# Performance work log

Hardware: AMD Instinct MI355X
Metric: run time of the kernel (lower is better)

## Reference

```python
import jax, jax.numpy as jnp
import numpy as np

NUM_EXPERTS = 64
TOPK = 2
N_TOKENS = 16384
DIM = 4096


def setup_inputs() -> dict:
    key = jax.random.key(0)
    k1, k2 = jax.random.split(key)
    x = jax.random.normal(k1, (N_TOKENS, DIM), dtype=jnp.float32)
    # gate weight, torch nn.Linear layout: [num_experts, dim], trunc-normal-ish small init
    W = jax.random.normal(k2, (NUM_EXPERTS, DIM), dtype=jnp.float32) * 0.02
    return {"x": x, "W": W}


def reference(x, W):
    # gate: logits = x @ W^T  -> [N, E]
    router_logits = x @ W.T
    # softmax computed in fp32 (matches dtype=torch.float32 in source)
    routing_weights = jax.nn.softmax(router_logits.astype(jnp.float32), axis=-1)
    # top-k experts per token
    top_w, selected_experts = jax.lax.top_k(routing_weights, TOPK)  # [N, k]
    top_w = top_w.astype(x.dtype)
    sel_flat = selected_experts.reshape(-1)  # [N*k]
    # histogram over experts (torch.histc with bins=num_experts)
    num_tokens_per_expert = jnp.bincount(sel_flat, length=NUM_EXPERTS)
    # stable argsort -> gather (permutation) indices grouping tokens by expert
    gather_indices = jnp.argsort(sel_flat, stable=True)
    return top_w.reshape(-1), gather_indices, num_tokens_per_expert
```

## Files before the change

### kernel.cpp

```cpp
#include <hip/hip_runtime.h>
#include <hip/hip_bf16.h>
#include <math.h>
#include <stdint.h>

#define N_TOKENS 16384
#define DIM 4096
#define NEXP 64

typedef const __attribute__((address_space(1))) void gvoid_t;
typedef __attribute__((address_space(3))) void svoid_t;
typedef short bf16x8 __attribute__((ext_vector_type(8)));
typedef float f32x4 __attribute__((ext_vector_type(4)));

constexpr int TOK_BLK = 32;

__device__ __forceinline__ unsigned short bf16_rn(float f) {
  unsigned u = __float_as_uint(f);
  u += 0x7fffu + ((u >> 16) & 1u);
  return (unsigned short)(u >> 16);
}
__device__ __forceinline__ float bf16_tof(unsigned short h) {
  return __uint_as_float(((unsigned)h) << 16);
}

__global__ __launch_bounds__(256) void k0_wsplit(const float* __restrict__ W,
                                                 unsigned short* __restrict__ hi,
                                                 unsigned short* __restrict__ lo,
                                                 int* __restrict__ cnt) {
  const int i = (blockIdx.x * 256 + threadIdx.x) * 4;
  const float4 f = *(const float4*)(W + i);
  ushort4 h, l;
  h.x = bf16_rn(f.x); l.x = bf16_rn(f.x - bf16_tof(h.x));
  h.y = bf16_rn(f.y); l.y = bf16_rn(f.y - bf16_tof(h.y));
  h.z = bf16_rn(f.z); l.z = bf16_rn(f.z - bf16_tof(h.z));
  h.w = bf16_rn(f.w); l.w = bf16_rn(f.w - bf16_tof(h.w));
  *(ushort4*)(hi + i) = h;
  *(ushort4*)(lo + i) = l;
  if (blockIdx.x < 8) {
    int4* c4 = (int4*)cnt;
    c4[blockIdx.x * 256 + threadIdx.x] = make_int4(0, 0, 0, 0);
  }
}

__global__ __launch_bounds__(256, 2) void k1_fused(
    const float* __restrict__ x, const unsigned short* __restrict__ Whi,
    const unsigned short* __restrict__ Wlo, float* __restrict__ topw,
    int* __restrict__ sel, int* __restrict__ cnt) {
  __shared__ unsigned short wh[2][NEXP * 64];
  __shared__ unsigned short wl[2][NEXP * 64];
  __shared__ float lg[TOK_BLK * 68];
  __shared__ int hist[NEXP];

  const int tid = threadIdx.x;
  const int lane = tid & 63;
  const int wid = __builtin_amdgcn_readfirstlane(tid >> 6);
  const int th = wid >> 1;
  const int eh = wid & 1;
  const int r = lane & 15;
  const int g = lane >> 4;
  const int tok0 = blockIdx.x * TOK_BLK;

  f32x4 acc[2] = {};

  auto stage_w = [&](unsigned short* hd, unsigned short* ld, int kc) {
#pragma unroll
    for (int q = 0; q < 2; ++q) {
      const int r0 = wid * 16 + q * 8;
      const int row = r0 + (lane >> 3);
      const int s = (lane & 7) ^ (row & 7);
      __builtin_amdgcn_global_load_lds((gvoid_t*)(Whi + (size_t)row * DIM + kc + 8 * s),
                                       (svoid_t*)(hd + r0 * 64), 16, 0, 0);
      __builtin_amdgcn_global_load_lds((gvoid_t*)(Wlo + (size_t)row * DIM + kc + 8 * s),
                                       (svoid_t*)(ld + r0 * 64), 16, 0, 0);
    }
  };

  const float* xrow = x + (size_t)(tok0 + th * 16 + r) * DIM + g * 8;

  auto xload = [&](float4* xd, int t) {
    const float* p = xrow + t * 64;
    xd[0] = *(const float4*)(p);
    xd[1] = *(const float4*)(p + 4);
    xd[2] = *(const float4*)(p + 32);
    xd[3] = *(const float4*)(p + 36);
  };

  auto body = [&](int t, float4* xc, float4* xn, unsigned short* whc,
                  unsigned short* wlc, unsigned short* whn, unsigned short* wln) {
    if (t + 1 < 64) {
      xload(xn, t + 1);
      stage_w(whn, wln, (t + 1) * 64);
    }
#pragma unroll
    for (int h = 0; h < 2; ++h) {
      const float fv[8] = {xc[2 * h].x, xc[2 * h].y, xc[2 * h].z, xc[2 * h].w,
                           xc[2 * h + 1].x, xc[2 * h + 1].y, xc[2 * h + 1].z,
                           xc[2 * h + 1].w};
      bf16x8 Ahi, Alo;
#pragma unroll
      for (int j = 0; j < 8; ++j) {
        const unsigned short hb = bf16_rn(fv[j]);
        Ahi[j] = (short)hb;
        Alo[j] = (short)bf16_rn(fv[j] - bf16_tof(hb));
      }
      const int ws = h * 4 + g;
#pragma unroll
      for (int nt = 0; nt < 2; ++nt) {
        const int wrow = eh * 32 + nt * 16 + r;
        const int wadr = wrow * 64 + 8 * (ws ^ (wrow & 7));
        const bf16x8 Bhi = *(const bf16x8*)(whc + wadr);
        const bf16x8 Blo = *(const bf16x8*)(wlc + wadr);
        acc[nt] = __builtin_amdgcn_mfma_f32_16x16x32_bf16(Ahi, Bhi, acc[nt], 0, 0, 0);
        acc[nt] = __builtin_amdgcn_mfma_f32_16x16x32_bf16(Alo, Bhi, acc[nt], 0, 0, 0);
        acc[nt] = __builtin_amdgcn_mfma_f32_16x16x32_bf16(Ahi, Blo, acc[nt], 0, 0, 0);
      }
    }
    __syncthreads();
  };

  float4 xA[4], xB[4];
  xload(xA, 0);
  stage_w(wh[0], wl[0], 0);
  __syncthreads();

  for (int tt = 0; tt < 64; tt += 2) {
    body(tt, xA, xB, wh[0], wl[0], wh[1], wl[1]);
    body(tt + 1, xB, xA, wh[1], wl[1], wh[0], wl[0]);
  }

  if (tid < NEXP) hist[tid] = 0;
#pragma unroll
  for (int nt = 0; nt < 2; ++nt)
#pragma unroll
    for (int rg = 0; rg < 4; ++rg)
      lg[(th * 16 + g * 4 + rg) * 68 + eh * 32 + nt * 16 + r] = acc[nt][rg];
  __syncthreads();

  if (tid < TOK_BLK) {
    const float* rowp = lg + tid * 68;
    float4 v[16];
#pragma unroll
    for (int c = 0; c < 16; ++c) v[c] = *(const float4*)(rowp + c * 4);

    float v0 = -INFINITY, v1 = -INFINITY;
    int i0 = 0, i1 = 0;
#define TOP2_STEP(val, idx)                                  \
  {                                                          \
    const float vv = (val);                                  \
    const int ee = (idx);                                    \
    if (vv > v0) { v1 = v0; i1 = i0; v0 = vv; i0 = ee; }     \
    else if (vv > v1) { v1 = vv; i1 = ee; }                  \
  }
#pragma unroll
    for (int c = 0; c < 16; ++c) {
      TOP2_STEP(v[c].x, c * 4 + 0);
      TOP2_STEP(v[c].y, c * 4 + 1);
      TOP2_STEP(v[c].z, c * 4 + 2);
      TOP2_STEP(v[c].w, c * 4 + 3);
    }
#undef TOP2_STEP

    float denom = 0.f;
#pragma unroll
    for (int c = 0; c < 16; ++c) {
      denom += expf(v[c].x - v0);
      denom += expf(v[c].y - v0);
      denom += expf(v[c].z - v0);
      denom += expf(v[c].w - v0);
    }
    const float w0 = 1.0f / denom;
    const float w1 = expf(v1 - v0) / denom;

    const int tk = tok0 + tid;
    topw[2 * tk + 0] = w0;
    topw[2 * tk + 1] = w1;
    sel[2 * tk + 0] = i0;
    sel[2 * tk + 1] = i1;
    atomicAdd(&hist[i0], 1);
    atomicAdd(&hist[i1], 1);
  }
  __syncthreads();
  if (tid < NEXP) {
    const int h = hist[tid];
    if (h) atomicAdd(&cnt[tid * 128 + (blockIdx.x >> 2)], h);
  }
}

__global__ void k3_scan(const int* __restrict__ cnt, int* __restrict__ cb,
                        float* __restrict__ counts_out) {
  __shared__ int tot[NEXP];
  const int e = threadIdx.x;
  const int4* row4 = (const int4*)(cnt + e * 128);
  int run = 0;
#pragma unroll
  for (int q = 0; q < 32; ++q) {
    const int4 v = row4[q];
    run += v.x + v.y + v.z + v.w;
  }
  tot[e] = run;
  counts_out[e] = (float)run;
  __syncthreads();
  int g = 0;
  for (int q = 0; q < e; ++q) g += tot[q];
  int r = g;
  for (int p = 0; p < 128; ++p) {
    cb[p * NEXP + e] = r;
    r += cnt[e * 128 + p];
  }
}

__global__ __launch_bounds__(256) void k4_scatter(const int* __restrict__ sel,
                                                  const int* __restrict__ cb,
                                                  float* __restrict__ gout) {
  __shared__ int wcnt[4 * NEXP];
  const int tid = threadIdx.x;
  const int s = blockIdx.x * 256 + tid;
  const int e = sel[s];
  const int lane = tid & 63;
  const int wv = tid >> 6;
  wcnt[tid] = 0;
  __syncthreads();

  unsigned long long mask = ~0ull;
#pragma unroll
  for (int b = 0; b < 6; ++b) {
    const unsigned long long bb = __ballot((e >> b) & 1);
    mask &= ((e >> b) & 1) ? bb : ~bb;
  }
  const unsigned long long below = mask & ((1ull << lane) - 1ull);
  const int wr = __popcll(below);
  if (wr == 0) wcnt[wv * NEXP + e] = __popcll(mask);
  __syncthreads();

  int base = cb[blockIdx.x * NEXP + e];
  for (int w2 = 0; w2 < wv; ++w2) base += wcnt[w2 * NEXP + e];
  gout[base + wr] = (float)s;
}

extern "C" void kernel_launch(void* const* d_in, const int* in_sizes, int n_in,
                              void* d_out, int out_size, void* d_ws, size_t ws_size,
                              hipStream_t stream) {
  const float* x = (const float*)d_in[0];
  const float* W = (const float*)d_in[1];
  float* out = (float*)d_out;

  unsigned short* whi_g = (unsigned short*)d_ws;
  unsigned short* wlo_g = whi_g + NEXP * DIM;
  int* sel = (int*)(wlo_g + NEXP * DIM);
  int* cnt = sel + N_TOKENS * 2;
  int* cb = cnt + 128 * NEXP;

  hipLaunchKernelGGL(k0_wsplit, dim3((NEXP * DIM) / 1024), dim3(256), 0, stream,
                     W, whi_g, wlo_g, cnt);
  hipLaunchKernelGGL(k1_fused, dim3(N_TOKENS / TOK_BLK), dim3(256), 0, stream,
                     x, whi_g, wlo_g, out, sel, cnt);
  hipLaunchKernelGGL(k3_scan, dim3(1), dim3(64), 0, stream, cnt, cb,
                     out + 2 * N_TOKENS + 2 * N_TOKENS);
  hipLaunchKernelGGL(k4_scatter, dim3((2 * N_TOKENS) / 256), dim3(256), 0, stream,
                     sel, cb, out + 2 * N_TOKENS);
}
```

Measured before the change: 114.2 us.

## Halve token block, give each wave one expert tile, share LDS, raise occupancy

Result: slower. 181.9 us (+59.3%).

```diff
diff --git a/kernel.cpp b/kernel.cpp
--- a/kernel.cpp
+++ b/kernel.cpp
@@ -12,7 +12,7 @@
 typedef short bf16x8 __attribute__((ext_vector_type(8)));
 typedef float f32x4 __attribute__((ext_vector_type(4)));
 
-constexpr int TOK_BLK = 32;
+constexpr int TOK_BLK = 16;
 
 __device__ __forceinline__ unsigned short bf16_rn(float f) {
   unsigned u = __float_as_uint(f);
@@ -21,6 +21,26 @@
 }
 __device__ __forceinline__ float bf16_tof(unsigned short h) {
   return __uint_as_float(((unsigned)h) << 16);
+}
+
+__device__ __forceinline__ void split8(const float4 a, const float4 b,
+                                       bf16x8& hi, bf16x8& lo) {
+  const float f[8] = {a.x, a.y, a.z, a.w, b.x, b.y, b.z, b.w};
+  union { unsigned u[4]; bf16x8 v; } H, L;
+#pragma unroll
+  for (int p = 0; p < 4; ++p) {
+    const float2 fp = make_float2(f[2 * p], f[2 * p + 1]);
+    const __hip_bfloat162 hh = __float22bfloat162_rn(fp);
+    const unsigned uh = *(const unsigned*)&hh;
+    const float h0 = __uint_as_float(uh << 16);
+    const float h1 = __uint_as_float(uh & 0xffff0000u);
+    const __hip_bfloat162 ll =
+        __float22bfloat162_rn(make_float2(fp.x - h0, fp.y - h1));
+    H.u[p] = uh;
+    L.u[p] = *(const unsigned*)&ll;
+  }
+  hi = H.v;
+  lo = L.v;
 }
 
 __global__ __launch_bounds__(256) void k0_wsplit(const float* __restrict__ W,
@@ -42,25 +62,26 @@
   }
 }
 
-__global__ __launch_bounds__(256, 2) void k1_fused(
+__global__ __launch_bounds__(256, 4) void k1_fused(
     const float* __restrict__ x, const unsigned short* __restrict__ Whi,
     const unsigned short* __restrict__ Wlo, float* __restrict__ topw,
     int* __restrict__ sel, int* __restrict__ cnt) {
-  __shared__ unsigned short wh[2][NEXP * 64];
-  __shared__ unsigned short wl[2][NEXP * 64];
-  __shared__ float lg[TOK_BLK * 68];
-  __shared__ int hist[NEXP];
+  __shared__ __align__(16) unsigned char smem[32768 + 256];
+  unsigned short* const wh0 = (unsigned short*)smem;
+  unsigned short* const wh1 = (unsigned short*)(smem + 8192);
+  unsigned short* const wl0 = (unsigned short*)(smem + 16384);
+  unsigned short* const wl1 = (unsigned short*)(smem + 24576);
+  float* const lg = (float*)smem;
+  int* const hist = (int*)(smem + 32768);
 
   const int tid = threadIdx.x;
   const int lane = tid & 63;
   const int wid = __builtin_amdgcn_readfirstlane(tid >> 6);
-  const int th = wid >> 1;
-  const int eh = wid & 1;
   const int r = lane & 15;
   const int g = lane >> 4;
   const int tok0 = blockIdx.x * TOK_BLK;
 
-  f32x4 acc[2] = {};
+  f32x4 acc = {};
 
   auto stage_w = [&](unsigned short* hd, unsigned short* ld, int kc) {
 #pragma unroll
@@ -68,15 +89,16 @@
       const int r0 = wid * 16 + q * 8;
       const int row = r0 + (lane >> 3);
       const int s = (lane & 7) ^ (row & 7);
-      __builtin_amdgcn_global_load_lds((gvoid_t*)(Whi + (size_t)row * DIM + kc + 8 * s),
-                                       (svoid_t*)(hd + r0 * 64), 16, 0, 0);
-      __builtin_amdgcn_global_load_lds((gvoid_t*)(Wlo + (size_t)row * DIM + kc + 8 * s),
-                                       (svoid_t*)(ld + r0 * 64), 16, 0, 0);
+      __builtin_amdgcn_global_load_lds(
+          (gvoid_t*)(Whi + (size_t)row * DIM + kc + 8 * s),
+          (svoid_t*)(hd + r0 * 64), 16, 0, 0);
+      __builtin_amdgcn_global_load_lds(
+          (gvoid_t*)(Wlo + (size_t)row * DIM + kc + 8 * s),
+          (svoid_t*)(ld + r0 * 64), 16, 0, 0);
     }
   };
 
-  const float* xrow = x + (size_t)(tok0 + th * 16 + r) * DIM + g * 8;
-
+  const float* xrow = x + (size_t)(tok0 + r) * DIM + g * 8;
   auto xload = [&](float4* xd, int t) {
     const float* p = xrow + t * 64;
     xd[0] = *(const float4*)(p);
@@ -93,47 +115,34 @@
     }
 #pragma unroll
     for (int h = 0; h < 2; ++h) {
-      const float fv[8] = {xc[2 * h].x, xc[2 * h].y, xc[2 * h].z, xc[2 * h].w,
-                           xc[2 * h + 1].x, xc[2 * h + 1].y, xc[2 * h + 1].z,
-                           xc[2 * h + 1].w};
       bf16x8 Ahi, Alo;
-#pragma unroll
-      for (int j = 0; j < 8; ++j) {
-        const unsigned short hb = bf16_rn(fv[j]);
-        Ahi[j] = (short)hb;
-        Alo[j] = (short)bf16_rn(fv[j] - bf16_tof(hb));
-      }
+      split8(xc[2 * h], xc[2 * h + 1], Ahi, Alo);
       const int ws = h * 4 + g;
-#pragma unroll
-      for (int nt = 0; nt < 2; ++nt) {
-        const int wrow = eh * 32 + nt * 16 + r;
-        const int wadr = wrow * 64 + 8 * (ws ^ (wrow & 7));
-        const bf16x8 Bhi = *(const bf16x8*)(whc + wadr);
-        const bf16x8 Blo = *(const bf16x8*)(wlc + wadr);
-        acc[nt] = __builtin_amdgcn_mfma_f32_16x16x32_bf16(Ahi, Bhi, acc[nt], 0, 0, 0);
-        acc[nt] = __builtin_amdgcn_mfma_f32_16x16x32_bf16(Alo, Bhi, acc[nt], 0, 0, 0);
-        acc[nt] = __builtin_amdgcn_mfma_f32_16x16x32_bf16(Ahi, Blo, acc[nt], 0, 0, 0);
-      }
+      const int wrow = wid * 16 + r;
+      const int wadr = wrow * 64 + 8 * (ws ^ (wrow & 7));
+      const bf16x8 Bhi = *(const bf16x8*)(whc + wadr);
+      const bf16x8 Blo = *(const bf16x8*)(wlc + wadr);
+      acc = __builtin_amdgcn_mfma_f32_16x16x32_bf16(Ahi, Bhi, acc, 0, 0, 0);
+      acc = __builtin_amdgcn_mfma_f32_16x16x32_bf16(Alo, Bhi, acc, 0, 0, 0);
+      acc = __builtin_amdgcn_mfma_f32_16x16x32_bf16(Ahi, Blo, acc, 0, 0, 0);
     }
     __syncthreads();
   };
 
   float4 xA[4], xB[4];
   xload(xA, 0);
-  stage_w(wh[0], wl[0], 0);
+  stage_w(wh0, wl0, 0);
   __syncthreads();
 
   for (int tt = 0; tt < 64; tt += 2) {
-    body(tt, xA, xB, wh[0], wl[0], wh[1], wl[1]);
-    body(tt + 1, xB, xA, wh[1], wl[1], wh[0], wl[0]);
+    body(tt, xA, xB, wh0, wl0, wh1, wl1);
+    body(tt + 1, xB, xA, wh1, wl1, wh0, wl0);
   }
 
   if (tid < NEXP) hist[tid] = 0;
 #pragma unroll
-  for (int nt = 0; nt < 2; ++nt)
-#pragma unroll
-    for (int rg = 0; rg < 4; ++rg)
-      lg[(th * 16 + g * 4 + rg) * 68 + eh * 32 + nt * 16 + r] = acc[nt][rg];
+  for (int rg = 0; rg < 4; ++rg)
+    lg[(g * 4 + rg) * 68 + wid * 16 + r] = acc[rg];
   __syncthreads();
 
   if (tid < TOK_BLK) {
@@ -182,7 +191,7 @@
   __syncthreads();
   if (tid < NEXP) {
     const int h = hist[tid];
-    if (h) atomicAdd(&cnt[tid * 128 + (blockIdx.x >> 2)], h);
+    if (h) atomicAdd(&cnt[tid * 128 + (blockIdx.x >> 3)], h);
   }
 }
 
```
